# Optimization experiments

Measured on AMD Instinct MI355X. Metric: run time of the kernel, lower is better.

## Reference

```python
import jax, jax.numpy as jnp
import numpy as np

N = 50000      # nodes
E = 800000     # edges (avg degree 16)
D = 128        # extended_lat_size = latent_size(124) + 4
G = 256        # number of graphs in the batch
H = 8 * D      # 1024, hidden width of MLP stack


def _w(k, shape):
    return jax.random.normal(k, shape, jnp.float32) * 0.02


def setup_inputs() -> dict:
    key = jax.random.key(0)
    ks = jax.random.split(key, 20)
    x = jax.random.normal(ks[0], (N, D), jnp.float32)
    edge_index = jax.random.randint(ks[1], (2, E), 0, N, dtype=jnp.int32)
    batch_vector = jnp.sort(jax.random.randint(ks[2], (N,), 0, G, dtype=jnp.int32))
    return {
        "x": x,
        "edge_index": edge_index,
        "batch_vector": batch_vector,
        # GCNConv layers
        "W1": _w(ks[3], (D, 2 * D)), "b1": jnp.zeros((2 * D,), jnp.float32),
        "W2": _w(ks[4], (2 * D, D)), "b2": jnp.zeros((D,), jnp.float32),
        # lazy Linear stack (in-dims resolved from dataflow)
        "Wl1": _w(ks[5], (D, D)),   "bl1": jnp.zeros((D,), jnp.float32),
        "Wl2": _w(ks[6], (D, H)),   "bl2": jnp.zeros((H,), jnp.float32),
        "Wl22": _w(ks[7], (H, H)),  "bl22": jnp.zeros((H,), jnp.float32),
        "Wl23": _w(ks[8], (H, H)),  "bl23": jnp.zeros((H,), jnp.float32),
        "Wl3": _w(ks[9], (H, D)),   "bl3": jnp.zeros((D,), jnp.float32),
    }


def gcn_conv(x, W, b, row, col):
    """PyG GCNConv: linear transform, add self-loops, symmetric norm, scatter-add."""
    h = x @ W  # [N, F_out]
    n = x.shape[0]
    loop = jnp.arange(n, dtype=row.dtype)
    r = jnp.concatenate([row, loop])   # source nodes
    c = jnp.concatenate([col, loop])   # target nodes
    deg = jax.ops.segment_sum(jnp.ones_like(c, dtype=h.dtype), c, num_segments=n)
    dinv = jnp.where(deg > 0, jax.lax.rsqrt(deg), 0.0)
    norm = dinv[r] * dinv[c]                         # [E+N]
    msg = h[r] * norm[:, None]                       # gather + scale
    out = jax.ops.segment_sum(msg, c, num_segments=n)  # scatter-add
    return out + b


def global_mean_pool(x, batch, num_graphs):
    s = jax.ops.segment_sum(x, batch, num_segments=num_graphs)
    cnt = jax.ops.segment_sum(jnp.ones((x.shape[0],), x.dtype), batch, num_segments=num_graphs)
    return s / jnp.maximum(cnt, 1.0)[:, None]


def reference(x, edge_index, batch_vector, W1, b1, W2, b2,
              Wl1, bl1, Wl2, bl2, Wl22, bl22, Wl23, bl23, Wl3, bl3):
    row, col = edge_index[0], edge_index[1]
    h = jax.nn.relu(gcn_conv(x, W1, b1, row, col))
    h = jax.nn.relu(gcn_conv(h, W2, b2, row, col))
    g = global_mean_pool(h, batch_vector, G)         # [G, D]
    g = jax.nn.relu(g @ Wl1 + bl1)
    g = jax.nn.relu(g @ Wl2 + bl2)
    g = jax.nn.relu(g @ Wl22 + bl22)
    g = jax.nn.relu(g @ Wl23 + bl23)
    g = g @ Wl3 + bl3                                 # [G, D]
    return jnp.squeeze(g).reshape(-1)                 # flatten -> [G*D]
```

## Files before the change

### kernel.cpp

```cpp
#include <hip/hip_runtime.h>


typedef __attribute__((ext_vector_type(8))) short bf16x8;
typedef __attribute__((ext_vector_type(8))) ushort u16x8;
typedef __attribute__((ext_vector_type(4))) float f32x4;

#define ADJ_STRIDE 64

__device__ __forceinline__ ushort f2bf(float f) {
    unsigned u = __float_as_uint(f);
    unsigned r = (u + 0x7FFFu + ((u >> 16) & 1u)) >> 16;
    return (ushort)r;
}
__device__ __forceinline__ float bf2f(ushort h) {
    return __uint_as_float(((unsigned)h) << 16);
}
__device__ __forceinline__ float bflo(unsigned u) {
    return __uint_as_float(u << 16);
}
__device__ __forceinline__ float bfhi(unsigned u) {
    return __uint_as_float(u & 0xffff0000u);
}
__device__ __forceinline__ void gload16(const ushort* g, ushort* l) {
    __builtin_amdgcn_global_load_lds(
        (const __attribute__((address_space(1))) void*)g,
        (__attribute__((address_space(3))) void*)l, 16, 0, 0);
}

#define SWZ(r) (((r) >> 1) & 3)


__global__ void fill_adj_fixed_kernel(const int* __restrict__ row,
                                      const int* __restrict__ col,
                                      int E, int N, int* __restrict__ indeg,
                                      int* __restrict__ adjf) {
    int r = blockIdx.x & 7, chunk = blockIdx.x >> 3;
    int lo = (int)(((long long)N * r) >> 3);
    int hi = (int)(((long long)N * (r + 1)) >> 3);
    int E4 = E >> 2;
#pragma unroll
    for (int v = 0; v < 2; ++v) {
        int i = chunk * 512 + v * 256 + threadIdx.x;
        if (i < E4) {
            int c0 = __builtin_nontemporal_load(col + i * 4 + 0);
            int c1 = __builtin_nontemporal_load(col + i * 4 + 1);
            int c2 = __builtin_nontemporal_load(col + i * 4 + 2);
            int c3 = __builtin_nontemporal_load(col + i * 4 + 3);
            int r0 = __builtin_nontemporal_load(row + i * 4 + 0);
            int r1 = __builtin_nontemporal_load(row + i * 4 + 1);
            int r2 = __builtin_nontemporal_load(row + i * 4 + 2);
            int r3 = __builtin_nontemporal_load(row + i * 4 + 3);
            if (c0 >= lo && c0 < hi) {
                int p = atomicAdd(&indeg[c0], 1);
                if (p < ADJ_STRIDE) adjf[(c0 << 6) + p] = r0;
            }
            if (c1 >= lo && c1 < hi) {
                int p = atomicAdd(&indeg[c1], 1);
                if (p < ADJ_STRIDE) adjf[(c1 << 6) + p] = r1;
            }
            if (c2 >= lo && c2 < hi) {
                int p = atomicAdd(&indeg[c2], 1);
                if (p < ADJ_STRIDE) adjf[(c2 << 6) + p] = r2;
            }
            if (c3 >= lo && c3 < hi) {
                int p = atomicAdd(&indeg[c3], 1);
                if (p < ADJ_STRIDE) adjf[(c3 << 6) + p] = r3;
            }
        }
    }
    if (blockIdx.x == 0 && threadIdx.x < (E & 3)) {
        int e = (E & ~3) + threadIdx.x;
        int c = col[e];
        int p = atomicAdd(&indeg[c], 1);
        if (p < ADJ_STRIDE) adjf[(c << 6) + p] = row[e];
    }
}

__global__ void dinv_kernel(const int* __restrict__ indeg, float* __restrict__ dinv,
                            int N) {
    int i = blockIdx.x * blockDim.x + threadIdx.x;
    if (i < N) dinv[i] = rsqrtf((float)(indeg[i] + 1));
}

struct TJobs {
    const float* W[7];
    ushort* Th[7];
    ushort* Tl[7];
    int K[7];
    int Nn[7];
    int off[8];
};

__global__ __launch_bounds__(256) void tsplit_all_kernel(TJobs jobs) {
    __shared__ float sm[64][65];
    int b = blockIdx.x;
    int j = 0;
#pragma unroll
    for (int t = 1; t < 7; ++t) if (b >= jobs.off[t]) j = t;
    int local = b - jobs.off[j];
    int K = jobs.K[j], Nn = jobs.Nn[j];
    int kt = K >> 6;
    int k0 = (local % kt) * 64, n0 = (local / kt) * 64;
    const float* W = jobs.W[j];
    ushort* Th = jobs.Th[j];
    ushort* Tl = jobs.Tl[j];

    int tid = threadIdx.x;
    int r = tid >> 2, cq = tid & 3;
#pragma unroll
    for (int i = 0; i < 4; ++i) {
        float4 v = *(const float4*)(W + (size_t)(k0 + r) * Nn + n0 + cq * 16 + i * 4);
        sm[r][cq * 16 + i * 4 + 0] = v.x;
        sm[r][cq * 16 + i * 4 + 1] = v.y;
        sm[r][cq * 16 + i * 4 + 2] = v.z;
        sm[r][cq * 16 + i * 4 + 3] = v.w;
    }
    __syncthreads();
    int n = tid >> 2, kq = tid & 3;
    ushort h[16], l[16];
#pragma unroll
    for (int i = 0; i < 16; ++i) {
        float v = sm[kq * 16 + i][n];
        h[i] = f2bf(v);
        l[i] = f2bf(v - bf2f(h[i]));
    }
    size_t o = (size_t)(n0 + n) * K + k0 + kq * 16;
    *(u16x8*)(&Th[o]) = *(u16x8*)&h[0];
    *(u16x8*)(&Th[o + 8]) = *(u16x8*)&h[8];
    *(u16x8*)(&Tl[o]) = *(u16x8*)&l[0];
    *(u16x8*)(&Tl[o + 8]) = *(u16x8*)&l[8];
}

__global__ void scale_to_bf16_kernel(const float* __restrict__ x,
                                     const float* __restrict__ dinv,
                                     ushort* __restrict__ xb, int total8) {
    int idx = blockIdx.x * blockDim.x + threadIdx.x;
    if (idx >= total8) return;
    float dv = dinv[idx >> 4];
    const float4* xp = (const float4*)x;
    float4 a = xp[idx * 2], b = xp[idx * 2 + 1];
    ushort h[8] = {f2bf(dv * a.x), f2bf(dv * a.y), f2bf(dv * a.z), f2bf(dv * a.w),
                   f2bf(dv * b.x), f2bf(dv * b.y), f2bf(dv * b.z), f2bf(dv * b.w)};
    *(u16x8*)(xb + (size_t)idx * 8) = *(u16x8*)&h[0];
}

template<int MODE>
__global__ void aggregate_bf16_kernel(const ushort* __restrict__ hsb,
                                      const int* __restrict__ indeg,
                                      const int* __restrict__ adjf,
                                      const float* __restrict__ dinv,
                                      const float* __restrict__ bias,
                                      float* __restrict__ outf,
                                      ushort* __restrict__ outh, ushort* __restrict__ outl,
                                      int N) {
    int wv = (blockIdx.x * blockDim.x + threadIdx.x) >> 6;
    int lane = threadIdx.x & 63;
    int half = lane >> 5, l32 = lane & 31;
    int node = wv * 2 + half;
    bool active = node < N;
    int nd = active ? node : N - 1;
    const uint2* base = (const uint2*)hsb;
    float dself = dinv[nd];
    uint2 sa = base[(size_t)nd * 32 + l32];
    float ax = bflo(sa.x), ay = bfhi(sa.x);
    float az = bflo(sa.y), aw = bfhi(sa.y);
    int s = nd << 6;
    int deg = active ? min(indeg[nd], ADJ_STRIDE) : 0;
    int mx = max(deg, __shfl_xor(deg, 32));
    for (int j = 0; j < mx; j += 16) {
        int idx[16]; float wgt[16];
#pragma unroll
        for (int k = 0; k < 16; ++k) {
            int jj = j + k;
            bool valid = jj < deg;
            int ld = adjf[s + (valid ? jj : 0)];
            idx[k] = valid ? ld : 0;
            wgt[k] = valid ? 1.f : 0.f;
        }
        uint2 v[16];
#pragma unroll
        for (int k = 0; k < 16; ++k) v[k] = base[(size_t)idx[k] * 32 + l32];
#pragma unroll
        for (int k = 0; k < 16; ++k) {
            ax = fmaf(wgt[k], bflo(v[k].x), ax);
            ay = fmaf(wgt[k], bfhi(v[k].x), ay);
            az = fmaf(wgt[k], bflo(v[k].y), az);
            aw = fmaf(wgt[k], bfhi(v[k].y), aw);
        }
    }
    ax *= dself; ay *= dself; az *= dself; aw *= dself;
    if (!active) return;
    if (MODE == 0) {
        float4 b = ((const float4*)bias)[l32];
        ax = fmaxf(ax + b.x, 0.f); ay = fmaxf(ay + b.y, 0.f);
        az = fmaxf(az + b.z, 0.f); aw = fmaxf(aw + b.w, 0.f);
        ((float4*)outf)[(size_t)node * 32 + l32] = make_float4(ax, ay, az, aw);
    } else {
        ushort h0 = f2bf(ax), h1 = f2bf(ay), h2 = f2bf(az), h3 = f2bf(aw);
        uint2 hv = make_uint2((unsigned)h0 | ((unsigned)h1 << 16),
                              (unsigned)h2 | ((unsigned)h3 << 16));
        ushort l0 = f2bf(ax - bf2f(h0)), l1 = f2bf(ay - bf2f(h1));
        ushort l2 = f2bf(az - bf2f(h2)), l3 = f2bf(aw - bf2f(h3));
        uint2 lv = make_uint2((unsigned)l0 | ((unsigned)l1 << 16),
                              (unsigned)l2 | ((unsigned)l3 << 16));
        ((uint2*)outh)[(size_t)node * 32 + l32] = hv;
        ((uint2*)outl)[(size_t)node * 32 + l32] = lv;
    }
}

__global__ __launch_bounds__(512) void gcn_mid_kernel(
        const ushort* __restrict__ Ah, const ushort* __restrict__ Al,
        const ushort* __restrict__ B1h, const ushort* __restrict__ B1l,
        const ushort* __restrict__ B2h, const ushort* __restrict__ B2l,
        const float* __restrict__ bias1, const float* __restrict__ dinv,
        ushort* __restrict__ outb, int M) {
    __shared__ __align__(16) ushort t1f[2 * 128 * 256 + 2 * 128 * 32];
    const int tid = threadIdx.x;
    const int w = tid >> 6, lane = tid & 63;
    const int bm = blockIdx.x * 128;
    const int sq = lane >> 4, r16 = lane & 15;

    {
        const int wr = w >> 2, wc = w & 3;
        f32x4 acc1[4][4];
#pragma unroll
        for (int i = 0; i < 4; ++i)
#pragma unroll
            for (int j = 0; j < 4; ++j) acc1[i][j] = (f32x4)0.f;

        for (int kk = 0; kk < 128; kk += 32) {
            {
                int rowi = w * 16 + (lane >> 2);
                int u = lane & 3;
                int colk = kk + 8 * (u ^ SWZ(rowi));
                gload16(Ah + (size_t)(bm + rowi) * 128 + colk, t1f + w * 512);
                gload16(Al + (size_t)(bm + rowi) * 128 + colk, t1f + 4096 + w * 512);
            }
#pragma unroll
            for (int v = 0; v < 2; ++v) {
                int chunk = v * 8 + w;
                int rowi = chunk * 16 + (lane >> 2);
                int u = lane & 3;
                int colk = kk + 8 * (u ^ SWZ(rowi));
                gload16(B1h + (size_t)rowi * 128 + colk, t1f + 8192 + chunk * 512);
                gload16(B1l + (size_t)rowi * 128 + colk, t1f + 16384 + chunk * 512);
            }
            __syncthreads();

            bf16x8 ah[4], al[4], bh[4], bl[4];
#pragma unroll
            for (int f = 0; f < 4; ++f) {
                int ra = wr * 64 + f * 16 + r16;
                int oa = ra * 32 + 8 * (sq ^ SWZ(ra));
                ah[f] = *(const bf16x8*)(t1f + oa);
                al[f] = *(const bf16x8*)(t1f + 4096 + oa);
                int rb = wc * 64 + f * 16 + r16;
                int ob = rb * 32 + 8 * (sq ^ SWZ(rb));
                bh[f] = *(const bf16x8*)(t1f + 8192 + ob);
                bl[f] = *(const bf16x8*)(t1f + 16384 + ob);
            }
#pragma unroll
            for (int i = 0; i < 4; ++i)
#pragma unroll
                for (int j = 0; j < 4; ++j) {
                    acc1[i][j] = __builtin_amdgcn_mfma_f32_16x16x32_bf16(ah[i], bh[j], acc1[i][j], 0, 0, 0);
                    acc1[i][j] = __builtin_amdgcn_mfma_f32_16x16x32_bf16(ah[i], bl[j], acc1[i][j], 0, 0, 0);
                    acc1[i][j] = __builtin_amdgcn_mfma_f32_16x16x32_bf16(al[i], bh[j], acc1[i][j], 0, 0, 0);
                }
            __syncthreads();
        }

        const int q4 = lane >> 4;
#pragma unroll
        for (int j = 0; j < 4; ++j) {
            int col = wc * 64 + j * 16 + r16;
            float bv = bias1[col];
            int cslot = col >> 3, coff = col & 7;
#pragma unroll
            for (int i = 0; i < 4; ++i) {
                int rowb = wr * 64 + i * 16 + q4 * 4;
#pragma unroll
                for (int r = 0; r < 4; ++r) {
                    int rowt = rowb + r;
                    float v = fmaxf(acc1[i][j][r] + bv, 0.f);
                    ushort h = f2bf(v);
                    ushort lo = f2bf(v - bf2f(h));
                    int a = rowt * 256 + (((cslot ^ (rowt & 7)) << 3) + coff);
                    t1f[a] = h;
                    t1f[32768 + a] = lo;
                }
            }
        }
    }

    {
        const int wr2 = w >> 1, wc2 = w & 1;
        const int q4 = lane >> 4;
        f32x4 acc2[2][4];
#pragma unroll
        for (int i = 0; i < 2; ++i)
#pragma unroll
            for (int j = 0; j < 4; ++j) acc2[i][j] = (f32x4)0.f;

        for (int kk = 0; kk < 256; kk += 32) {
            {
                int rowi = w * 16 + (lane >> 2);
                int u = lane & 3;
                int colk = kk + 8 * (u ^ SWZ(rowi));
                gload16(B2h + (size_t)rowi * 256 + colk, t1f + 65536 + w * 512);
                gload16(B2l + (size_t)rowi * 256 + colk, t1f + 69632 + w * 512);
            }
            __syncthreads();

            bf16x8 a2h[2], a2l[2], b2h[4], b2l[4];
#pragma unroll
            for (int f = 0; f < 2; ++f) {
                int ra = wr2 * 32 + f * 16 + r16;
                int k0 = kk + sq * 8;
                int ao = ra * 256 + (((k0 >> 3) ^ (ra & 7)) << 3);
                a2h[f] = *(const bf16x8*)(t1f + ao);
                a2l[f] = *(const bf16x8*)(t1f + 32768 + ao);
            }
#pragma unroll
            for (int f = 0; f < 4; ++f) {
                int rb = wc2 * 64 + f * 16 + r16;
                int ob = rb * 32 + 8 * (sq ^ SWZ(rb));
                b2h[f] = *(const bf16x8*)(t1f + 65536 + ob);
                b2l[f] = *(const bf16x8*)(t1f + 69632 + ob);
            }
#pragma unroll
            for (int i = 0; i < 2; ++i)
#pragma unroll
                for (int j = 0; j < 4; ++j) {
                    acc2[i][j] = __builtin_amdgcn_mfma_f32_16x16x32_bf16(a2h[i], b2h[j], acc2[i][j], 0, 0, 0);
                    acc2[i][j] = __builtin_amdgcn_mfma_f32_16x16x32_bf16(a2h[i], b2l[j], acc2[i][j], 0, 0, 0);
                    acc2[i][j] = __builtin_amdgcn_mfma_f32_16x16x32_bf16(a2l[i], b2h[j], acc2[i][j], 0, 0, 0);
                }
            __syncthreads();
        }

#pragma unroll
        for (int i = 0; i < 2; ++i) {
            int row0 = bm + wr2 * 32 + i * 16 + q4 * 4;
            if (row0 >= M) continue;
#pragma unroll
            for (int j = 0; j < 4; ++j) {
                int col = wc2 * 64 + j * 16 + r16;
#pragma unroll
                for (int r = 0; r < 4; ++r)
                    outb[(size_t)(row0 + r) * 128 + col] =
                        f2bf(acc2[i][j][r] * dinv[row0 + r]);
            }
        }
    }
}

template<int BM, int BN, int EPI>
__global__ __launch_bounds__(256) void gemm_bf16x3_kernel(
        const ushort* __restrict__ Ah, const ushort* __restrict__ Al,
        const ushort* __restrict__ Bth, const ushort* __restrict__ Btl,
        const float* __restrict__ bias, const float* __restrict__ rowscale,
        float* __restrict__ Cf, ushort* __restrict__ Ch, ushort* __restrict__ Cl,
        int M, int N, int K, int kChunk) {
    constexpr int WMm = BM / 2, WMn = BN / 2;
    constexpr int FRm = WMm / 16, FRn = WMn / 16;
    __shared__ __align__(16) ushort lds[(2 * BM + 2 * BN) * 32];
    const int tbB[4] = {0, BM * 64, 2 * BM * 64, (2 * BM + BN) * 64};

    const int tid = threadIdx.x;
    const int w = tid >> 6, lane = tid & 63;
    const int wr = w >> 1, wc = w & 1;
    const int bm = blockIdx.x * BM, bn = blockIdx.y * BN;
    const int k0 = blockIdx.z * kChunk;
    int k1 = k0 + kChunk; if (k1 > K) k1 = K;

    const ushort* srcs[4] = {
        Ah  + (size_t)bm * K, Al  + (size_t)bm * K,
        Bth + (size_t)bn * K, Btl + (size_t)bn * K };

    f32x4 acc[FRm][FRn];
#pragma unroll
    for (int i = 0; i < FRm; ++i)
#pragma unroll
        for (int j = 0; j < FRn; ++j) acc[i][j] = (f32x4)0.f;

    const int sq = lane >> 4, r16 = lane & 15;

    for (int kk = k0; kk < k1; kk += 32) {
#pragma unroll
        for (int t = 0; t < 4; ++t) {
            const int rows = (t < 2) ? BM : BN;
            const int nv = rows / 64;
#pragma unroll
            for (int v = 0; v < nv; ++v) {
                int chunk = v * 4 + w;
                int rowi = chunk * 16 + (lane >> 2);
                int u = lane & 3;
                int colk = kk + 8 * (u ^ SWZ(rowi));
                const ushort* g = srcs[t] + (size_t)rowi * K + colk;
                ushort* lp = (ushort*)((char*)lds + tbB[t] + chunk * 16 * 64);
                gload16(g, lp);
            }
        }
        __syncthreads();

        bf16x8 ah[FRm], al[FRm], bh[FRn], bl[FRn];
#pragma unroll
        for (int f = 0; f < FRm; ++f) {
            int ra = wr * WMm + f * 16 + r16;
            int oa = ra * 64 + 16 * (sq ^ SWZ(ra));
            ah[f] = *(const bf16x8*)((const char*)lds + tbB[0] + oa);
            al[f] = *(const bf16x8*)((const char*)lds + tbB[1] + oa);
        }
#pragma unroll
        for (int f = 0; f < FRn; ++f) {
            int rb = wc * WMn + f * 16 + r16;
            int ob = rb * 64 + 16 * (sq ^ SWZ(rb));
            bh[f] = *(const bf16x8*)((const char*)lds + tbB[2] + ob);
            bl[f] = *(const bf16x8*)((const char*)lds + tbB[3] + ob);
        }

#pragma unroll
        for (int i = 0; i < FRm; ++i)
#pragma unroll
            for (int j = 0; j < FRn; ++j) {
                acc[i][j] = __builtin_amdgcn_mfma_f32_16x16x32_bf16(ah[i], bh[j], acc[i][j], 0, 0, 0);
                acc[i][j] = __builtin_amdgcn_mfma_f32_16x16x32_bf16(ah[i], bl[j], acc[i][j], 0, 0, 0);
                acc[i][j] = __builtin_amdgcn_mfma_f32_16x16x32_bf16(al[i], bh[j], acc[i][j], 0, 0, 0);
            }
        __syncthreads();
    }

    const int q4 = lane >> 4;
#pragma unroll
    for (int i = 0; i < FRm; ++i) {
        int row0 = bm + wr * WMm + i * 16 + q4 * 4;
        if (row0 >= M) continue;
#pragma unroll
        for (int j = 0; j < FRn; ++j) {
            int colc = bn + wc * WMn + j * 16 + r16;
            if (EPI == 1) {
                float bv = bias[colc];
#pragma unroll
                for (int r = 0; r < 4; ++r) {
                    float v = fmaxf(acc[i][j][r] + bv, 0.f);
                    ushort h = f2bf(v);
                    ushort lo = f2bf(v - bf2f(h));
                    size_t o = (size_t)(row0 + r) * N + colc;
                    Ch[o] = h; Cl[o] = lo;
                }
            } else if (EPI == 0) {
#pragma unroll
                for (int r = 0; r < 4; ++r) {
                    float v = acc[i][j][r] * rowscale[row0 + r];
                    Cf[(size_t)(row0 + r) * N + colc] = v;
                }
            } else {
#pragma unroll
                for (int r = 0; r < 4; ++r)
                    atomicAdd(&Cf[(size_t)(row0 + r) * N + colc], acc[i][j][r]);
            }
        }
    }
}

__global__ void finish_kernel(const float* __restrict__ acc, const float* __restrict__ bias,
                              float* __restrict__ outf, ushort* __restrict__ outh,
                              ushort* __restrict__ outl, int total, int Ncols, int doRelu) {
    int idx = blockIdx.x * blockDim.x + threadIdx.x;
    if (idx >= total) return;
    float v = acc[idx] + bias[idx & (Ncols - 1)];
    if (doRelu) v = fmaxf(v, 0.f);
    if (outh) {
        ushort h = f2bf(v);
        outh[idx] = h;
        outl[idx] = f2bf(v - bf2f(h));
    } else {
        outf[idx] = v;
    }
}

__global__ void pool_kernel(const float* __restrict__ feats, const int* __restrict__ batch,
                            ushort* __restrict__ gh, ushort* __restrict__ gl, int N) {
    __shared__ float sm[256];
    int gid = blockIdx.x;
    int lo = 0, hi = N;
    while (lo < hi) { int m = (lo + hi) >> 1; if (batch[m] < gid) lo = m + 1; else hi = m; }
    int start = lo;
    lo = start; hi = N;
    while (lo < hi) { int m = (lo + hi) >> 1; if (batch[m] < gid + 1) lo = m + 1; else hi = m; }
    int end = lo;
    int tid = threadIdx.x;
    int f = tid & 127, half = tid >> 7;
    float acc = 0.f;
    for (int i = start + half; i < end; i += 2) acc += feats[(size_t)i * 128 + f];
    sm[tid] = acc;
    __syncthreads();
    if (half == 0) {
        acc += sm[tid + 128];
        int cnt = end - start; if (cnt < 1) cnt = 1;
        float m = acc / (float)cnt;
        ushort h = f2bf(m);
        gh[gid * 128 + f] = h;
        gl[gid * 128 + f] = f2bf(m - bf2f(h));
    }
}


extern "C" void kernel_launch(void* const* d_in, const int* in_sizes, int n_in,
                              void* d_out, int out_size, void* d_ws, size_t ws_size,
                              hipStream_t stream) {
    const float* x    = (const float*)d_in[0];
    const int*   ei   = (const int*)d_in[1];
    const int*   batch= (const int*)d_in[2];
    const float* W1   = (const float*)d_in[3];
    const float* b1   = (const float*)d_in[4];
    const float* W2   = (const float*)d_in[5];
    const float* b2   = (const float*)d_in[6];
    const float* Wl1  = (const float*)d_in[7];
    const float* bl1  = (const float*)d_in[8];
    const float* Wl2  = (const float*)d_in[9];
    const float* bl2  = (const float*)d_in[10];
    const float* Wl22 = (const float*)d_in[11];
    const float* bl22 = (const float*)d_in[12];
    const float* Wl23 = (const float*)d_in[13];
    const float* bl23 = (const float*)d_in[14];
    const float* Wl3  = (const float*)d_in[15];
    const float* bl3  = (const float*)d_in[16];

    const int D = 128;
    const int N = in_sizes[0] / D;
    const int E = in_sizes[1] / 2;
    const int G = out_size / D;
    const int H = in_sizes[10];
    const int Mpad = ((N + 127) / 128) * 128;
    const int* row = ei;
    const int* col = ei + E;
    float* out = (float*)d_out;

    char* ws = (char*)d_ws;
    auto alloc = [&](size_t bytes) -> void* {
        void* p = (void*)ws;
        ws += (bytes + 255) & ~(size_t)255;
        return p;
    };
    int*    indeg  = (int*)alloc((size_t)N * 4);
    int*    adjf   = (int*)alloc((size_t)N * ADJ_STRIDE * 4);
    float*  dinv   = (float*)alloc((size_t)N * 4);
    ushort* W1th   = (ushort*)alloc((size_t)256 * 128 * 2);
    ushort* W1tl   = (ushort*)alloc((size_t)256 * 128 * 2);
    ushort* W2th   = (ushort*)alloc((size_t)128 * 256 * 2);
    ushort* W2tl   = (ushort*)alloc((size_t)128 * 256 * 2);
    ushort* Tl1h  = (ushort*)alloc((size_t)128 * 128 * 2);
    ushort* Tl1l  = (ushort*)alloc((size_t)128 * 128 * 2);
    ushort* Tl2h  = (ushort*)alloc((size_t)H * 128 * 2);
    ushort* Tl2l  = (ushort*)alloc((size_t)H * 128 * 2);
    ushort* Tl22h = (ushort*)alloc((size_t)H * H * 2);
    ushort* Tl22l = (ushort*)alloc((size_t)H * H * 2);
    ushort* Tl23h = (ushort*)alloc((size_t)H * H * 2);
    ushort* Tl23l = (ushort*)alloc((size_t)H * H * 2);
    ushort* Tl3h  = (ushort*)alloc((size_t)128 * H * 2);
    ushort* Tl3l  = (ushort*)alloc((size_t)128 * H * 2);
    ushort* xb     = (ushort*)alloc((size_t)Mpad * 128 * 2);
    ushort* yh     = (ushort*)alloc((size_t)Mpad * 128 * 2);
    ushort* yl     = (ushort*)alloc((size_t)Mpad * 128 * 2);
    ushort* hs2b   = (ushort*)alloc((size_t)Mpad * 128 * 2);
    float*  yf     = (float*)alloc((size_t)Mpad * 128 * 4);
    ushort* gh     = (ushort*)alloc((size_t)G * 128 * 2);
    ushort* gl     = (ushort*)alloc((size_t)G * 128 * 2);
    ushort* a1h    = (ushort*)alloc((size_t)G * 128 * 2);
    ushort* a1l    = (ushort*)alloc((size_t)G * 128 * 2);
    ushort* a2h    = (ushort*)alloc((size_t)G * H * 2);
    ushort* a2l    = (ushort*)alloc((size_t)G * H * 2);
    ushort* a3h    = (ushort*)alloc((size_t)G * H * 2);
    ushort* a3l    = (ushort*)alloc((size_t)G * H * 2);
    ushort* a4h    = (ushort*)alloc((size_t)G * H * 2);
    ushort* a4l    = (ushort*)alloc((size_t)G * H * 2);
    float*  accb   = (float*)alloc((size_t)G * H * 4);
    float*  accf   = (float*)alloc((size_t)G * 128 * 4);

    const int CHUNKS = (E / 4 + 511) / 512;
    hipMemsetAsync(indeg, 0, (size_t)N * 4, stream);
    fill_adj_fixed_kernel<<<8 * CHUNKS, 256, 0, stream>>>(row, col, E, N, indeg, adjf);
    dinv_kernel<<<(N + 255) / 256, 256, 0, stream>>>(indeg, dinv, N);

    {
        TJobs jb;
        const float* Ws[7]  = {W1, W2, Wl1, Wl2, Wl22, Wl23, Wl3};
        ushort* Ths[7]      = {W1th, W2th, Tl1h, Tl2h, Tl22h, Tl23h, Tl3h};
        ushort* Tls[7]      = {W1tl, W2tl, Tl1l, Tl2l, Tl22l, Tl23l, Tl3l};
        int Ks[7]           = {128, 256, 128, 128, H, H, H};
        int Nns[7]          = {256, 128, 128, H, H, H, 128};
        int off = 0;
        for (int j = 0; j < 7; ++j) {
            jb.W[j] = Ws[j]; jb.Th[j] = Ths[j]; jb.Tl[j] = Tls[j];
            jb.K[j] = Ks[j]; jb.Nn[j] = Nns[j];
            jb.off[j] = off;
            off += (Ks[j] / 64) * (Nns[j] / 64);
        }
        jb.off[7] = off;
        tsplit_all_kernel<<<off, 256, 0, stream>>>(jb);
    }

    scale_to_bf16_kernel<<<(N * 16 + 255) / 256, 256, 0, stream>>>(x, dinv, xb, N * 16);

    aggregate_bf16_kernel<1><<<(N + 7) / 8, 256, 0, stream>>>(
        xb, indeg, adjf, dinv, nullptr, nullptr, yh, yl, N);

    gcn_mid_kernel<<<Mpad / 128, 512, 0, stream>>>(
        yh, yl, W1th, W1tl, W2th, W2tl, b1, dinv, hs2b, N);

    aggregate_bf16_kernel<0><<<(N + 7) / 8, 256, 0, stream>>>(
        hs2b, indeg, adjf, dinv, b2, yf, nullptr, nullptr, N);

    pool_kernel<<<G, 256, 0, stream>>>(yf, batch, gh, gl, N);

    {
        dim3 grid(G / 64, 2);
        gemm_bf16x3_kernel<64, 64, 1><<<grid, 256, 0, stream>>>(
            gh, gl, Tl1h, Tl1l, bl1, nullptr, nullptr, a1h, a1l, G, 128, 128, 128);
    }
    {
        dim3 grid(G / 64, H / 64);
        gemm_bf16x3_kernel<64, 64, 1><<<grid, 256, 0, stream>>>(
            a1h, a1l, Tl2h, Tl2l, bl2, nullptr, nullptr, a2h, a2l, G, H, 128, 128);
    }
    {
        hipMemsetAsync(accb, 0, (size_t)G * H * 4, stream);
        dim3 grid(G / 64, H / 64, 4);
        gemm_bf16x3_kernel<64, 64, 3><<<grid, 256, 0, stream>>>(
            a2h, a2l, Tl22h, Tl22l, nullptr, nullptr, accb, nullptr, nullptr, G, H, H, 256);
        finish_kernel<<<(G * H + 255) / 256, 256, 0, stream>>>(
            accb, bl22, nullptr, a3h, a3l, G * H, H, 1);
    }
    {
        hipMemsetAsync(accb, 0, (size_t)G * H * 4, stream);
        dim3 grid(G / 64, H / 64, 4);
        gemm_bf16x3_kernel<64, 64, 3><<<grid, 256, 0, stream>>>(
            a3h, a3l, Tl23h, Tl23l, nullptr, nullptr, accb, nullptr, nullptr, G, H, H, 256);
        finish_kernel<<<(G * H + 255) / 256, 256, 0, stream>>>(
            accb, bl23, nullptr, a4h, a4l, G * H, H, 1);
    }
    {
        hipMemsetAsync(accf, 0, (size_t)G * 128 * 4, stream);
        dim3 grid(G / 64, 2, 8);
        gemm_bf16x3_kernel<64, 64, 3><<<grid, 256, 0, stream>>>(
            a4h, a4l, Tl3h, Tl3l, nullptr, nullptr, accf, nullptr, nullptr, G, 128, H, 128);
        finish_kernel<<<(G * 128 + 255) / 256, 256, 0, stream>>>(
            accf, bl3, out, nullptr, nullptr, G * 128, 128, 0);
    }
}
```

Measured before the change: 248.6 us.

## Merge preprocessing kernels into one launch and batch accumulator memsets

Adjacency fill, weight transpose/split, and the x-to-bf16 conversion now run as one combined kernel that dispatches on block index. The dinv scaling of source features moves out of the conversion and into the first aggregation, which multiplies each gathered neighbour by its dinv. The three accumulator memsets become a single upfront memset, using a second buffer so accb is not reused between layers. This removes several launches and serialization points, at the cost of an extra dinv gather per neighbour in aggregation and a relies-on-contiguous-allocation memset.

```diff
diff --git a/kernel.cpp b/kernel.cpp
--- a/kernel.cpp
+++ b/kernel.cpp
@@ -29,50 +29,118 @@
 
 #define SWZ(r) (((r) >> 1) & 3)
 
-
-__global__ void fill_adj_fixed_kernel(const int* __restrict__ row,
-                                      const int* __restrict__ col,
-                                      int E, int N, int* __restrict__ indeg,
-                                      int* __restrict__ adjf) {
-    int r = blockIdx.x & 7, chunk = blockIdx.x >> 3;
-    int lo = (int)(((long long)N * r) >> 3);
-    int hi = (int)(((long long)N * (r + 1)) >> 3);
-    int E4 = E >> 2;
-#pragma unroll
-    for (int v = 0; v < 2; ++v) {
-        int i = chunk * 512 + v * 256 + threadIdx.x;
-        if (i < E4) {
-            int c0 = __builtin_nontemporal_load(col + i * 4 + 0);
-            int c1 = __builtin_nontemporal_load(col + i * 4 + 1);
-            int c2 = __builtin_nontemporal_load(col + i * 4 + 2);
-            int c3 = __builtin_nontemporal_load(col + i * 4 + 3);
-            int r0 = __builtin_nontemporal_load(row + i * 4 + 0);
-            int r1 = __builtin_nontemporal_load(row + i * 4 + 1);
-            int r2 = __builtin_nontemporal_load(row + i * 4 + 2);
-            int r3 = __builtin_nontemporal_load(row + i * 4 + 3);
-            if (c0 >= lo && c0 < hi) {
-                int p = atomicAdd(&indeg[c0], 1);
-                if (p < ADJ_STRIDE) adjf[(c0 << 6) + p] = r0;
-            }
-            if (c1 >= lo && c1 < hi) {
-                int p = atomicAdd(&indeg[c1], 1);
-                if (p < ADJ_STRIDE) adjf[(c1 << 6) + p] = r1;
-            }
-            if (c2 >= lo && c2 < hi) {
-                int p = atomicAdd(&indeg[c2], 1);
-                if (p < ADJ_STRIDE) adjf[(c2 << 6) + p] = r2;
-            }
-            if (c3 >= lo && c3 < hi) {
-                int p = atomicAdd(&indeg[c3], 1);
-                if (p < ADJ_STRIDE) adjf[(c3 << 6) + p] = r3;
-            }
-        }
-    }
-    if (blockIdx.x == 0 && threadIdx.x < (E & 3)) {
-        int e = (E & ~3) + threadIdx.x;
-        int c = col[e];
-        int p = atomicAdd(&indeg[c], 1);
-        if (p < ADJ_STRIDE) adjf[(c << 6) + p] = row[e];
+struct PreArgs {
+    const int* row;
+    const int* col;
+    int E, N;
+    int* indeg;
+    int* adjf;
+    const float* W[7];
+    ushort* Th[7];
+    ushort* Tl[7];
+    int K[7], Nn[7], off[8];
+    const float* x;
+    ushort* xb;
+    int total8;
+    int nFill, nT;
+};
+
+__global__ __launch_bounds__(256) void preproc_mega_kernel(PreArgs a) {
+    __shared__ float sm[64][65];
+    int bid = blockIdx.x;
+    int tid = threadIdx.x;
+
+    if (bid < a.nFill) {
+        int r = bid & 7, chunk = bid >> 3;
+        int lo = (int)(((long long)a.N * r) >> 3);
+        int hi = (int)(((long long)a.N * (r + 1)) >> 3);
+        int E4 = a.E >> 2;
+#pragma unroll
+        for (int v = 0; v < 2; ++v) {
+            int i = chunk * 512 + v * 256 + tid;
+            if (i < E4) {
+                int c0 = __builtin_nontemporal_load(a.col + i * 4 + 0);
+                int c1 = __builtin_nontemporal_load(a.col + i * 4 + 1);
+                int c2 = __builtin_nontemporal_load(a.col + i * 4 + 2);
+                int c3 = __builtin_nontemporal_load(a.col + i * 4 + 3);
+                int r0 = __builtin_nontemporal_load(a.row + i * 4 + 0);
+                int r1 = __builtin_nontemporal_load(a.row + i * 4 + 1);
+                int r2 = __builtin_nontemporal_load(a.row + i * 4 + 2);
+                int r3 = __builtin_nontemporal_load(a.row + i * 4 + 3);
+                if (c0 >= lo && c0 < hi) {
+                    int p = atomicAdd(&a.indeg[c0], 1);
+                    if (p < ADJ_STRIDE) a.adjf[(c0 << 6) + p] = r0;
+                }
+                if (c1 >= lo && c1 < hi) {
+                    int p = atomicAdd(&a.indeg[c1], 1);
+                    if (p < ADJ_STRIDE) a.adjf[(c1 << 6) + p] = r1;
+                }
+                if (c2 >= lo && c2 < hi) {
+                    int p = atomicAdd(&a.indeg[c2], 1);
+                    if (p < ADJ_STRIDE) a.adjf[(c2 << 6) + p] = r2;
+                }
+                if (c3 >= lo && c3 < hi) {
+                    int p = atomicAdd(&a.indeg[c3], 1);
+                    if (p < ADJ_STRIDE) a.adjf[(c3 << 6) + p] = r3;
+                }
+            }
+        }
+        if (bid == 0 && tid < (a.E & 3)) {
+            int e = (a.E & ~3) + tid;
+            int c = a.col[e];
+            int p = atomicAdd(&a.indeg[c], 1);
+            if (p < ADJ_STRIDE) a.adjf[(c << 6) + p] = a.row[e];
+        }
+        return;
+    }
+
+    if (bid < a.nFill + a.nT) {
+        int b = bid - a.nFill;
+        int j = 0;
+#pragma unroll
+        for (int t = 1; t < 7; ++t) if (b >= a.off[t]) j = t;
+        int local = b - a.off[j];
+        int K = a.K[j], Nn = a.Nn[j];
+        int kt = K >> 6;
+        int k0 = (local % kt) * 64, n0 = (local / kt) * 64;
+        const float* W = a.W[j];
+        ushort* Th = a.Th[j];
+        ushort* Tl = a.Tl[j];
+
+        int r = tid >> 2, cq = tid & 3;
+#pragma unroll
+        for (int i = 0; i < 4; ++i) {
+            float4 v = *(const float4*)(W + (size_t)(k0 + r) * Nn + n0 + cq * 16 + i * 4);
+            sm[r][cq * 16 + i * 4 + 0] = v.x;
+            sm[r][cq * 16 + i * 4 + 1] = v.y;
+            sm[r][cq * 16 + i * 4 + 2] = v.z;
+            sm[r][cq * 16 + i * 4 + 3] = v.w;
+        }
+        __syncthreads();
+        int n = tid >> 2, kq = tid & 3;
+        ushort h[16], l[16];
+#pragma unroll
+        for (int i = 0; i < 16; ++i) {
+            float v = sm[kq * 16 + i][n];
+            h[i] = f2bf(v);
+            l[i] = f2bf(v - bf2f(h[i]));
+        }
+        size_t o = (size_t)(n0 + n) * K + k0 + kq * 16;
+        *(u16x8*)(&Th[o]) = *(u16x8*)&h[0];
+        *(u16x8*)(&Th[o + 8]) = *(u16x8*)&h[8];
+        *(u16x8*)(&Tl[o]) = *(u16x8*)&l[0];
+        *(u16x8*)(&Tl[o + 8]) = *(u16x8*)&l[8];
+        return;
+    }
+
+    {
+        int idx = (bid - a.nFill - a.nT) * 256 + tid;
+        if (idx >= a.total8) return;
+        const float4* xp = (const float4*)a.x;
+        float4 v0 = xp[idx * 2], v1 = xp[idx * 2 + 1];
+        ushort h[8] = {f2bf(v0.x), f2bf(v0.y), f2bf(v0.z), f2bf(v0.w),
+                       f2bf(v1.x), f2bf(v1.y), f2bf(v1.z), f2bf(v1.w)};
+        *(u16x8*)(a.xb + (size_t)idx * 8) = *(u16x8*)&h[0];
     }
 }
 
@@ -80,68 +148,6 @@
                             int N) {
     int i = blockIdx.x * blockDim.x + threadIdx.x;
     if (i < N) dinv[i] = rsqrtf((float)(indeg[i] + 1));
-}
-
-struct TJobs {
-    const float* W[7];
-    ushort* Th[7];
-    ushort* Tl[7];
-    int K[7];
-    int Nn[7];
-    int off[8];
-};
-
-__global__ __launch_bounds__(256) void tsplit_all_kernel(TJobs jobs) {
-    __shared__ float sm[64][65];
-    int b = blockIdx.x;
-    int j = 0;
-#pragma unroll
-    for (int t = 1; t < 7; ++t) if (b >= jobs.off[t]) j = t;
-    int local = b - jobs.off[j];
-    int K = jobs.K[j], Nn = jobs.Nn[j];
-    int kt = K >> 6;
-    int k0 = (local % kt) * 64, n0 = (local / kt) * 64;
-    const float* W = jobs.W[j];
-    ushort* Th = jobs.Th[j];
-    ushort* Tl = jobs.Tl[j];
-
-    int tid = threadIdx.x;
-    int r = tid >> 2, cq = tid & 3;
-#pragma unroll
-    for (int i = 0; i < 4; ++i) {
-        float4 v = *(const float4*)(W + (size_t)(k0 + r) * Nn + n0 + cq * 16 + i * 4);
-        sm[r][cq * 16 + i * 4 + 0] = v.x;
-        sm[r][cq * 16 + i * 4 + 1] = v.y;
-        sm[r][cq * 16 + i * 4 + 2] = v.z;
-        sm[r][cq * 16 + i * 4 + 3] = v.w;
-    }
-    __syncthreads();
-    int n = tid >> 2, kq = tid & 3;
-    ushort h[16], l[16];
-#pragma unroll
-    for (int i = 0; i < 16; ++i) {
-        float v = sm[kq * 16 + i][n];
-        h[i] = f2bf(v);
-        l[i] = f2bf(v - bf2f(h[i]));
-    }
-    size_t o = (size_t)(n0 + n) * K + k0 + kq * 16;
-    *(u16x8*)(&Th[o]) = *(u16x8*)&h[0];
-    *(u16x8*)(&Th[o + 8]) = *(u16x8*)&h[8];
-    *(u16x8*)(&Tl[o]) = *(u16x8*)&l[0];
-    *(u16x8*)(&Tl[o + 8]) = *(u16x8*)&l[8];
-}
-
-__global__ void scale_to_bf16_kernel(const float* __restrict__ x,
-                                     const float* __restrict__ dinv,
-                                     ushort* __restrict__ xb, int total8) {
-    int idx = blockIdx.x * blockDim.x + threadIdx.x;
-    if (idx >= total8) return;
-    float dv = dinv[idx >> 4];
-    const float4* xp = (const float4*)x;
-    float4 a = xp[idx * 2], b = xp[idx * 2 + 1];
-    ushort h[8] = {f2bf(dv * a.x), f2bf(dv * a.y), f2bf(dv * a.z), f2bf(dv * a.w),
-                   f2bf(dv * b.x), f2bf(dv * b.y), f2bf(dv * b.z), f2bf(dv * b.w)};
-    *(u16x8*)(xb + (size_t)idx * 8) = *(u16x8*)&h[0];
 }
 
 template<int MODE>
@@ -162,8 +168,9 @@
     const uint2* base = (const uint2*)hsb;
     float dself = dinv[nd];
     uint2 sa = base[(size_t)nd * 32 + l32];
-    float ax = bflo(sa.x), ay = bfhi(sa.x);
-    float az = bflo(sa.y), aw = bfhi(sa.y);
+    float sw = (MODE == 1) ? dself : 1.f;
+    float ax = sw * bflo(sa.x), ay = sw * bfhi(sa.x);
+    float az = sw * bflo(sa.y), aw = sw * bfhi(sa.y);
     int s = nd << 6;
     int deg = active ? min(indeg[nd], ADJ_STRIDE) : 0;
     int mx = max(deg, __shfl_xor(deg, 32));
@@ -180,6 +187,10 @@
         uint2 v[16];
 #pragma unroll
         for (int k = 0; k < 16; ++k) v[k] = base[(size_t)idx[k] * 32 + l32];
+        if (MODE == 1) {
+#pragma unroll
+            for (int k = 0; k < 16; ++k) wgt[k] *= dinv[idx[k]];
+        }
 #pragma unroll
         for (int k = 0; k < 16; ++k) {
             ax = fmaf(wgt[k], bflo(v[k].x), ax);
@@ -577,15 +588,17 @@
     ushort* a4h    = (ushort*)alloc((size_t)G * H * 2);
     ushort* a4l    = (ushort*)alloc((size_t)G * H * 2);
     float*  accb   = (float*)alloc((size_t)G * H * 4);
+    float*  accb2  = (float*)alloc((size_t)G * H * 4);
     float*  accf   = (float*)alloc((size_t)G * 128 * 4);
 
+    hipMemsetAsync(indeg, 0, (size_t)N * 4, stream);
+    hipMemsetAsync(accb, 0, ((size_t)2 * G * H + G * 128) * 4, stream);
+
     const int CHUNKS = (E / 4 + 511) / 512;
-    hipMemsetAsync(indeg, 0, (size_t)N * 4, stream);
-    fill_adj_fixed_kernel<<<8 * CHUNKS, 256, 0, stream>>>(row, col, E, N, indeg, adjf);
-    dinv_kernel<<<(N + 255) / 256, 256, 0, stream>>>(indeg, dinv, N);
-
-    {
-        TJobs jb;
+    {
+        PreArgs pa;
+        pa.row = row; pa.col = col; pa.E = E; pa.N = N;
+        pa.indeg = indeg; pa.adjf = adjf;
         const float* Ws[7]  = {W1, W2, Wl1, Wl2, Wl22, Wl23, Wl3};
         ushort* Ths[7]      = {W1th, W2th, Tl1h, Tl2h, Tl22h, Tl23h, Tl3h};
         ushort* Tls[7]      = {W1tl, W2tl, Tl1l, Tl2l, Tl22l, Tl23l, Tl3l};
@@ -593,16 +606,19 @@
         int Nns[7]          = {256, 128, 128, H, H, H, 128};
         int off = 0;
         for (int j = 0; j < 7; ++j) {
-            jb.W[j] = Ws[j]; jb.Th[j] = Ths[j]; jb.Tl[j] = Tls[j];
-            jb.K[j] = Ks[j]; jb.Nn[j] = Nns[j];
-            jb.off[j] = off;
+            pa.W[j] = Ws[j]; pa.Th[j] = Ths[j]; pa.Tl[j] = Tls[j];
+            pa.K[j] = Ks[j]; pa.Nn[j] = Nns[j];
+            pa.off[j] = off;
             off += (Ks[j] / 64) * (Nns[j] / 64);
         }
-        jb.off[7] = off;
-        tsplit_all_kernel<<<off, 256, 0, stream>>>(jb);
-    }
-
-    scale_to_bf16_kernel<<<(N * 16 + 255) / 256, 256, 0, stream>>>(x, dinv, xb, N * 16);
+        pa.off[7] = off;
+        pa.x = x; pa.xb = xb; pa.total8 = N * 16;
+        pa.nFill = 8 * CHUNKS;
+        pa.nT = off;
+        int nCvt = (pa.total8 + 255) / 256;
+        preproc_mega_kernel<<<pa.nFill + pa.nT + nCvt, 256, 0, stream>>>(pa);
+    }
+    dinv_kernel<<<(N + 255) / 256, 256, 0, stream>>>(indeg, dinv, N);
 
     aggregate_bf16_kernel<1><<<(N + 7) / 8, 256, 0, stream>>>(
         xb, indeg, adjf, dinv, nullptr, nullptr, yh, yl, N);
@@ -626,7 +642,6 @@
             a1h, a1l, Tl2h, Tl2l, bl2, nullptr, nullptr, a2h, a2l, G, H, 128, 128);
     }
     {
-        hipMemsetAsync(accb, 0, (size_t)G * H * 4, stream);
         dim3 grid(G / 64, H / 64, 4);
         gemm_bf16x3_kernel<64, 64, 3><<<grid, 256, 0, stream>>>(
             a2h, a2l, Tl22h, Tl22l, nullptr, nullptr, accb, nullptr, nullptr, G, H, H, 256);
@@ -634,15 +649,13 @@
             accb, bl22, nullptr, a3h, a3l, G * H, H, 1);
     }
     {
-        hipMemsetAsync(accb, 0, (size_t)G * H * 4, stream);
         dim3 grid(G / 64, H / 64, 4);
         gemm_bf16x3_kernel<64, 64, 3><<<grid, 256, 0, stream>>>(
-            a3h, a3l, Tl23h, Tl23l, nullptr, nullptr, accb, nullptr, nullptr, G, H, H, 256);
+            a3h, a3l, Tl23h, Tl23l, nullptr, nullptr, accb2, nullptr, nullptr, G, H, H, 256);
         finish_kernel<<<(G * H + 255) / 256, 256, 0, stream>>>(
-            accb, bl23, nullptr, a4h, a4l, G * H, H, 1);
-    }
-    {
-        hipMemsetAsync(accf, 0, (size_t)G * 128 * 4, stream);
+            accb2, bl23, nullptr, a4h, a4l, G * H, H, 1);
+    }
+    {
         dim3 grid(G / 64, 2, 8);
         gemm_bf16x3_kernel<64, 64, 3><<<grid, 256, 0, stream>>>(
             a4h, a4l, Tl3h, Tl3l, nullptr, nullptr, accf, nullptr, nullptr, G, 128, H, 128);
```

After: 242.5 us, median of 2. 2.4% less time.
